# Optimization experiments

Hardware: AMD Instinct MI355X
Metric: run time of the kernel (lower is better)

The kernel has to match this reference:

```python
import jax, jax.numpy as jnp
import numpy as np

BATCH, SEQ_LEN, VOCAB, DIM = 64, 512, 32000, 512


def setup_inputs() -> dict:
    key = jax.random.key(0)
    k = jax.random.split(key, 6)
    s = 1.0 / np.sqrt(DIM)
    return {
        "x": jax.random.randint(k[0], (BATCH, SEQ_LEN), 0, VOCAB),
        "emb": jax.random.normal(k[1], (VOCAB, DIM), dtype=jnp.float32),
        "W_ih": jax.random.normal(k[2], (DIM, DIM), dtype=jnp.float32) * s,
        "W_hh": jax.random.normal(k[3], (DIM, DIM), dtype=jnp.float32) * s,
        "b_ih": jax.random.normal(k[4], (DIM,), dtype=jnp.float32) * s,
        "b_hh": jax.random.normal(k[5], (DIM,), dtype=jnp.float32) * s,
    }


def reference(x, emb, W_ih, W_hh, b_ih, b_hh):
    # Embedding lookup: [B, T, I]
    xe = emb[x]
    # Precompute input projections for all timesteps: [T, B, H]
    xp = jnp.einsum("bti,hi->tbh", xe, W_ih) + b_ih + b_hh
    h0 = jnp.zeros((x.shape[0], W_hh.shape[0]), dtype=xe.dtype)

    def step(h, xp_t):
        h_new = jnp.tanh(xp_t + h @ W_hh.T)
        return h_new, h_new

    _, hiddens = jax.lax.scan(step, h0, xp)  # [T, B, H]
    hiddens = jnp.transpose(hiddens, (1, 2, 0))  # [B, H, T]
    return jax.nn.softmax(hiddens, axis=1)
```

## Files before the change

kernel.cpp:

```cpp
#include <hip/hip_runtime.h>
#include <cstdint>

#define BATCH 64
#define SEQ   512
#define DIM   512
#define MTOT  (BATCH*SEQ)

#define CSL 8
#define GRP 32
#define RPG 2
#define SLOT (GRP*RPG*DIM)

__global__ __launch_bounds__(128) void pack_w(const float* __restrict__ W,
                                              float4* __restrict__ Wpk,
                                              unsigned long long* __restrict__ hpair) {
    const int c  = blockIdx.x;
    const int jb = threadIdx.x;
    const float4 v = *(const float4*)&W[(size_t)c * DIM + 4 * jb];
    Wpk[(size_t)jb * DIM + c] = v;
    hpair[(size_t)blockIdx.x * 128 + threadIdx.x] = 0ull;
}

__global__ __launch_bounds__(256) void embed_proj(
    const int*   __restrict__ xidx,
    const float* __restrict__ emb,
    const float* __restrict__ W_ih,
    const float* __restrict__ b_ih,
    const float* __restrict__ b_hh,
    float*       __restrict__ xp) {
    __shared__ float As[64][68];
    __shared__ float Bs[64][68];

    const int m0  = blockIdx.x * 64;
    const int n0  = blockIdx.y * 64;
    const int tid = threadIdx.x;

    const int lr = tid >> 4;
    const int lc = (tid & 15) << 2;

    int rows[4];
#pragma unroll
    for (int i = 0; i < 4; i++) rows[i] = xidx[m0 + lr + 16 * i];

    const int tm = (tid & 15) << 2;
    const int tn = (tid >> 4) << 2;

    float acc[4][4];
#pragma unroll
    for (int i = 0; i < 4; i++)
#pragma unroll
        for (int j = 0; j < 4; j++) acc[i][j] = 0.0f;

    for (int k0 = 0; k0 < DIM; k0 += 64) {
#pragma unroll
        for (int i = 0; i < 4; i++) {
            const int rl = lr + 16 * i;
            const float4 a = *(const float4*)&emb[(size_t)rows[i] * DIM + k0 + lc];
            As[lc + 0][rl] = a.x; As[lc + 1][rl] = a.y;
            As[lc + 2][rl] = a.z; As[lc + 3][rl] = a.w;
            const float4 b = *(const float4*)&W_ih[(size_t)(n0 + rl) * DIM + k0 + lc];
            Bs[lc + 0][rl] = b.x; Bs[lc + 1][rl] = b.y;
            Bs[lc + 2][rl] = b.z; Bs[lc + 3][rl] = b.w;
        }
        __syncthreads();
#pragma unroll 8
        for (int kk = 0; kk < 64; kk++) {
            const float4 a = *(const float4*)&As[kk][tm];
            const float4 b = *(const float4*)&Bs[kk][tn];
            acc[0][0] = fmaf(a.x, b.x, acc[0][0]);
            acc[0][1] = fmaf(a.x, b.y, acc[0][1]);
            acc[0][2] = fmaf(a.x, b.z, acc[0][2]);
            acc[0][3] = fmaf(a.x, b.w, acc[0][3]);
            acc[1][0] = fmaf(a.y, b.x, acc[1][0]);
            acc[1][1] = fmaf(a.y, b.y, acc[1][1]);
            acc[1][2] = fmaf(a.y, b.z, acc[1][2]);
            acc[1][3] = fmaf(a.y, b.w, acc[1][3]);
            acc[2][0] = fmaf(a.z, b.x, acc[2][0]);
            acc[2][1] = fmaf(a.z, b.y, acc[2][1]);
            acc[2][2] = fmaf(a.z, b.z, acc[2][2]);
            acc[2][3] = fmaf(a.z, b.w, acc[2][3]);
            acc[3][0] = fmaf(a.w, b.x, acc[3][0]);
            acc[3][1] = fmaf(a.w, b.y, acc[3][1]);
            acc[3][2] = fmaf(a.w, b.z, acc[3][2]);
            acc[3][3] = fmaf(a.w, b.w, acc[3][3]);
        }
        __syncthreads();
    }

    const int n = n0 + tn;
    const float bias0 = b_ih[n + 0] + b_hh[n + 0];
    const float bias1 = b_ih[n + 1] + b_hh[n + 1];
    const float bias2 = b_ih[n + 2] + b_hh[n + 2];
    const float bias3 = b_ih[n + 3] + b_hh[n + 3];
#pragma unroll
    for (int i = 0; i < 4; i++) {
        float4 o;
        o.x = acc[i][0] + bias0;
        o.y = acc[i][1] + bias1;
        o.z = acc[i][2] + bias2;
        o.w = acc[i][3] + bias3;
        *(float4*)&xp[(size_t)(m0 + tm + i) * DIM + n] = o;
    }
}

__global__ __launch_bounds__(512, 2)
void rnn_scan(const float4* __restrict__ Wpk, float* __restrict__ buf,
              unsigned long long* __restrict__ hpair) {
    __shared__ float hlds[RPG][DIM];
    __shared__ float part[2][RPG][8][64];

    const int tid   = threadIdx.x;
    const int slice = blockIdx.x / GRP;
    const int grp   = blockIdx.x % GRP;
    const int c     = tid & 63;
    const int ks    = tid >> 6;
    const int b0    = grp * RPG;
    const int col0  = slice * 64;
    const int hb    = ks * 16;

    float4 wreg[16];
#pragma unroll
    for (int i = 0; i < 16; i++)
        wreg[i] = Wpk[(size_t)(hb + i) * DIM + col0 + c];

    hlds[0][tid] = 0.0f;
    hlds[1][tid] = 0.0f;
    asm volatile("" ::: "memory");

    const unsigned long long* const pollb =
        hpair + (size_t)grp * (RPG * DIM) + tid;

    const int rr = tid >> 6;
    const int cc = tid & 63;
    float xq = 0.0f;
    size_t bufoff = 0;
    unsigned long long* pubp = nullptr;
    if (tid < 128) {
        bufoff = (size_t)(b0 + rr) * SEQ * DIM + col0 + cc;
        xq     = buf[bufoff];
        pubp   = hpair + ((size_t)grp * RPG + rr) * DIM + col0 + cc;
    }

    for (int t = 0; t < SEQ; t++) {
#pragma unroll
        for (int i = 0; i < 16; i++)
            asm volatile("" : "+v"(wreg[i].x), "+v"(wreg[i].y),
                              "+v"(wreg[i].z), "+v"(wreg[i].w));

        if (t > 0) {
            const unsigned long long* bp = pollb + (size_t)(t & 1) * SLOT;
            const unsigned tgt = (unsigned)t;
            unsigned long long v0 = __hip_atomic_load(bp, __ATOMIC_RELAXED,
                                                      __HIP_MEMORY_SCOPE_AGENT);
            unsigned long long v1 = __hip_atomic_load(bp + DIM, __ATOMIC_RELAXED,
                                                      __HIP_MEMORY_SCOPE_AGENT);
            int spins = 0;
            while (((unsigned)(v0 >> 32) != tgt) |
                   ((unsigned)(v1 >> 32) != tgt)) {
                if (++spins > 16) __builtin_amdgcn_s_sleep(1);
                v0 = __hip_atomic_load(bp, __ATOMIC_RELAXED,
                                       __HIP_MEMORY_SCOPE_AGENT);
                v1 = __hip_atomic_load(bp + DIM, __ATOMIC_RELAXED,
                                       __HIP_MEMORY_SCOPE_AGENT);
            }
            hlds[0][tid] = __uint_as_float((unsigned)v0);
            hlds[1][tid] = __uint_as_float((unsigned)v1);
            asm volatile("" ::: "memory");
        }

        float p0 = 0.f, p1 = 0.f;
        const float4* h40 = (const float4*)&hlds[0][0];
        const float4* h41 = (const float4*)&hlds[1][0];
#pragma unroll
        for (int i = 0; i < 16; i++) {
            const float4 w = wreg[i];
            const float4 a = h40[hb + i];
            const float4 b = h41[hb + i];
            p0 = fmaf(w.x, a.x, p0); p0 = fmaf(w.y, a.y, p0);
            p0 = fmaf(w.z, a.z, p0); p0 = fmaf(w.w, a.w, p0);
            p1 = fmaf(w.x, b.x, p1); p1 = fmaf(w.y, b.y, p1);
            p1 = fmaf(w.z, b.z, p1); p1 = fmaf(w.w, b.w, p1);
        }

        const int p = t & 1;
        part[p][0][ks][c] = p0;
        part[p][1][ks][c] = p1;
        __syncthreads();

        if (tid < 128) {
            float s = part[p][rr][0][cc];
#pragma unroll
            for (int k = 1; k < 8; k++) s += part[p][rr][k][cc];
            const float hn = tanhf(xq + s);
            if (t + 1 < SEQ) {
                const unsigned long long pv =
                    ((unsigned long long)(unsigned)(t + 1) << 32) |
                    (unsigned long long)__float_as_uint(hn);
                __hip_atomic_store(pubp + (size_t)((t + 1) & 1) * SLOT, pv,
                                   __ATOMIC_RELAXED, __HIP_MEMORY_SCOPE_AGENT);
            }
            buf[bufoff + (size_t)t * DIM] = hn;
            const int tn2 = (t + 1 < SEQ) ? (t + 1) : t;
            xq = buf[bufoff + (size_t)tn2 * DIM];
        }
    }
}

__global__ __launch_bounds__(256) void softmax_T(const float* __restrict__ hid,
                                                 float* __restrict__ out) {
    __shared__ float rowmax[64];
    __shared__ float rowinv[64];
    __shared__ float tile[64][65];

    const int b   = blockIdx.x;
    const int t0  = blockIdx.y * 64;
    const int tid = threadIdx.x;
    const float* base = hid + ((size_t)b * SEQ + t0) * DIM;

    const int r = tid >> 2;
    const int p = tid & 3;

    float m = -1e30f;
#pragma unroll 4
    for (int k = 0; k < 32; k++) {
        const float4 v = *(const float4*)&base[r * DIM + ((k * 4 + p) << 2)];
        m = fmaxf(m, fmaxf(fmaxf(v.x, v.y), fmaxf(v.z, v.w)));
    }
    m = fmaxf(m, __shfl_xor(m, 1));
    m = fmaxf(m, __shfl_xor(m, 2));

    float s = 0.0f;
#pragma unroll 4
    for (int k = 0; k < 32; k++) {
        const float4 v = *(const float4*)&base[r * DIM + ((k * 4 + p) << 2)];
        s += expf(v.x - m) + expf(v.y - m) + expf(v.z - m) + expf(v.w - m);
    }
    s += __shfl_xor(s, 1);
    s += __shfl_xor(s, 2);
    if (p == 0) {
        rowmax[r] = m;
        rowinv[r] = 1.0f / s;
    }
    __syncthreads();

    for (int hc = 0; hc < 8; hc++) {
#pragma unroll
        for (int i = 0; i < 16; i++) {
            const int lin = tid + 256 * i;
            const int rrr = lin >> 6;
            const int ccc = lin & 63;
            const float v = base[rrr * DIM + hc * 64 + ccc];
            tile[ccc][rrr] = expf(v - rowmax[rrr]) * rowinv[rrr];
        }
        __syncthreads();
#pragma unroll
        for (int i = 0; i < 16; i++) {
            const int lin = tid + 256 * i;
            const int hh  = lin >> 6;
            const int tt  = lin & 63;
            out[((size_t)b * DIM + hc * 64 + hh) * SEQ + t0 + tt] = tile[hh][tt];
        }
        __syncthreads();
    }
}

extern "C" void kernel_launch(void* const* d_in, const int* in_sizes, int n_in,
                              void* d_out, int out_size, void* d_ws, size_t ws_size,
                              hipStream_t stream) {
    const int*   x    = (const int*)  d_in[0];
    const float* emb  = (const float*)d_in[1];
    const float* W_ih = (const float*)d_in[2];
    const float* W_hh = (const float*)d_in[3];
    const float* b_ih = (const float*)d_in[4];
    const float* b_hh = (const float*)d_in[5];
    float* out = (float*)d_out;

    float* buf = (float*)d_ws;
    float4* Wpk = (float4*)out;
    unsigned long long* hpair =
        (unsigned long long*)(out + (4 << 20));

    pack_w<<<dim3(DIM), 128, 0, stream>>>(W_hh, Wpk, hpair);
    embed_proj<<<dim3(MTOT / 64, DIM / 64), 256, 0, stream>>>(x, emb, W_ih, b_ih, b_hh, buf);
    rnn_scan<<<CSL * GRP, 512, 0, stream>>>(Wpk, buf, hpair);
    softmax_T<<<dim3(BATCH, SEQ / 64), 256, 0, stream>>>(buf, out);
}
```

Baseline: 1.268 ms.

## Split RNN step per batch row to overlap row-B polling with row-A compute

```diff
diff --git a/kernel.cpp b/kernel.cpp
--- a/kernel.cpp
+++ b/kernel.cpp
@@ -107,7 +107,7 @@
 void rnn_scan(const float4* __restrict__ Wpk, float* __restrict__ buf,
               unsigned long long* __restrict__ hpair) {
     __shared__ float hlds[RPG][DIM];
-    __shared__ float part[2][RPG][8][64];
+    __shared__ float part[RPG][8][64];
 
     const int tid   = threadIdx.x;
     const int slice = blockIdx.x / GRP;
@@ -117,6 +117,7 @@
     const int b0    = grp * RPG;
     const int col0  = slice * 64;
     const int hb    = ks * 16;
+    const int wid   = ks;
 
     float4 wreg[16];
 #pragma unroll
@@ -127,70 +128,104 @@
     hlds[1][tid] = 0.0f;
     asm volatile("" ::: "memory");
 
-    const unsigned long long* const pollb =
-        hpair + (size_t)grp * (RPG * DIM) + tid;
-
-    const int rr = tid >> 6;
-    const int cc = tid & 63;
+    unsigned long long* const gbase = hpair + (size_t)grp * (RPG * DIM);
+
     float xq = 0.0f;
     size_t bufoff = 0;
     unsigned long long* pubp = nullptr;
-    if (tid < 128) {
-        bufoff = (size_t)(b0 + rr) * SEQ * DIM + col0 + cc;
+    if (wid < RPG) {
+        bufoff = (size_t)(b0 + wid) * SEQ * DIM + col0 + c;
         xq     = buf[bufoff];
-        pubp   = hpair + ((size_t)grp * RPG + rr) * DIM + col0 + cc;
-    }
+        pubp   = hpair + ((size_t)grp * RPG + wid) * DIM + col0 + c;
+    }
+
+    unsigned long long pendA = 0, pendB = 0;
 
     for (int t = 0; t < SEQ; t++) {
-#pragma unroll
-        for (int i = 0; i < 16; i++)
-            asm volatile("" : "+v"(wreg[i].x), "+v"(wreg[i].y),
-                              "+v"(wreg[i].z), "+v"(wreg[i].w));
+        const unsigned tgt = (unsigned)t;
 
         if (t > 0) {
-            const unsigned long long* bp = pollb + (size_t)(t & 1) * SLOT;
-            const unsigned tgt = (unsigned)t;
-            unsigned long long v0 = __hip_atomic_load(bp, __ATOMIC_RELAXED,
-                                                      __HIP_MEMORY_SCOPE_AGENT);
-            unsigned long long v1 = __hip_atomic_load(bp + DIM, __ATOMIC_RELAXED,
-                                                      __HIP_MEMORY_SCOPE_AGENT);
+            const unsigned long long* bp = gbase + (size_t)(t & 1) * SLOT + tid;
+            unsigned long long v = pendA;
             int spins = 0;
-            while (((unsigned)(v0 >> 32) != tgt) |
-                   ((unsigned)(v1 >> 32) != tgt)) {
+            while ((unsigned)(v >> 32) != tgt) {
                 if (++spins > 16) __builtin_amdgcn_s_sleep(1);
-                v0 = __hip_atomic_load(bp, __ATOMIC_RELAXED,
-                                       __HIP_MEMORY_SCOPE_AGENT);
-                v1 = __hip_atomic_load(bp + DIM, __ATOMIC_RELAXED,
-                                       __HIP_MEMORY_SCOPE_AGENT);
-            }
-            hlds[0][tid] = __uint_as_float((unsigned)v0);
-            hlds[1][tid] = __uint_as_float((unsigned)v1);
+                v = __hip_atomic_load(bp, __ATOMIC_RELAXED,
+                                      __HIP_MEMORY_SCOPE_AGENT);
+            }
+            hlds[0][tid] = __uint_as_float((unsigned)v);
             asm volatile("" ::: "memory");
-        }
-
-        float p0 = 0.f, p1 = 0.f;
-        const float4* h40 = (const float4*)&hlds[0][0];
-        const float4* h41 = (const float4*)&hlds[1][0];
-#pragma unroll
-        for (int i = 0; i < 16; i++) {
-            const float4 w = wreg[i];
-            const float4 a = h40[hb + i];
-            const float4 b = h41[hb + i];
-            p0 = fmaf(w.x, a.x, p0); p0 = fmaf(w.y, a.y, p0);
-            p0 = fmaf(w.z, a.z, p0); p0 = fmaf(w.w, a.w, p0);
-            p1 = fmaf(w.x, b.x, p1); p1 = fmaf(w.y, b.y, p1);
-            p1 = fmaf(w.z, b.z, p1); p1 = fmaf(w.w, b.w, p1);
-        }
-
-        const int p = t & 1;
-        part[p][0][ks][c] = p0;
-        part[p][1][ks][c] = p1;
-        __syncthreads();
-
-        if (tid < 128) {
-            float s = part[p][rr][0][cc];
-#pragma unroll
-            for (int k = 1; k < 8; k++) s += part[p][rr][k][cc];
+            pendB = __hip_atomic_load(bp + DIM, __ATOMIC_RELAXED,
+                                      __HIP_MEMORY_SCOPE_AGENT);
+        }
+
+        {
+            float p = 0.f;
+            const float4* h4 = (const float4*)&hlds[0][0];
+#pragma unroll
+            for (int i = 0; i < 16; i++) {
+                const float4 w = wreg[i];
+                const float4 a = h4[hb + i];
+                p = fmaf(w.x, a.x, p); p = fmaf(w.y, a.y, p);
+                p = fmaf(w.z, a.z, p); p = fmaf(w.w, a.w, p);
+            }
+            part[0][ks][c] = p;
+        }
+        __syncthreads();
+
+        if (wid == 0) {
+            float s = part[0][0][c];
+#pragma unroll
+            for (int k = 1; k < 8; k++) s += part[0][k][c];
+            const float hn = tanhf(xq + s);
+            if (t + 1 < SEQ) {
+                const unsigned long long pv =
+                    ((unsigned long long)(unsigned)(t + 1) << 32) |
+                    (unsigned long long)__float_as_uint(hn);
+                __hip_atomic_store(pubp + (size_t)((t + 1) & 1) * SLOT, pv,
+                                   __ATOMIC_RELAXED, __HIP_MEMORY_SCOPE_AGENT);
+            }
+            buf[bufoff + (size_t)t * DIM] = hn;
+            const int tn2 = (t + 1 < SEQ) ? (t + 1) : t;
+            xq = buf[bufoff + (size_t)tn2 * DIM];
+        }
+
+        if (t > 0) {
+            const unsigned long long* bp =
+                gbase + (size_t)(t & 1) * SLOT + DIM + tid;
+            unsigned long long v = pendB;
+            int spins = 0;
+            while ((unsigned)(v >> 32) != tgt) {
+                if (++spins > 16) __builtin_amdgcn_s_sleep(1);
+                v = __hip_atomic_load(bp, __ATOMIC_RELAXED,
+                                      __HIP_MEMORY_SCOPE_AGENT);
+            }
+            hlds[1][tid] = __uint_as_float((unsigned)v);
+            asm volatile("" ::: "memory");
+        }
+
+        {
+            float p = 0.f;
+            const float4* h4 = (const float4*)&hlds[1][0];
+#pragma unroll
+            for (int i = 0; i < 16; i++) {
+                const float4 w = wreg[i];
+                const float4 a = h4[hb + i];
+                p = fmaf(w.x, a.x, p); p = fmaf(w.y, a.y, p);
+                p = fmaf(w.z, a.z, p); p = fmaf(w.w, a.w, p);
+            }
+            part[1][ks][c] = p;
+        }
+        if (t + 1 < SEQ)
+            pendA = __hip_atomic_load(
+                gbase + (size_t)((t + 1) & 1) * SLOT + tid,
+                __ATOMIC_RELAXED, __HIP_MEMORY_SCOPE_AGENT);
+        __syncthreads();
+
+        if (wid == 1) {
+            float s = part[1][0][c];
+#pragma unroll
+            for (int k = 1; k < 8; k++) s += part[1][k][c];
             const float hn = tanhf(xq + s);
             if (t + 1 < SEQ) {
                 const unsigned long long pv =
```

After: 1.269 ms. Within noise of the previous version (+0.1%).

## Repartition RNN scan into 16 column slices and pipeline rows per block

Applied to the files above, without the earlier changes.

```diff
diff --git a/kernel.cpp b/kernel.cpp
--- a/kernel.cpp
+++ b/kernel.cpp
@@ -6,9 +6,9 @@
 #define DIM   512
 #define MTOT  (BATCH*SEQ)
 
-#define CSL 8
-#define GRP 32
-#define RPG 2
+#define CSL 16
+#define GRP 16
+#define RPG 4
 #define SLOT (GRP*RPG*DIM)
 
 __global__ __launch_bounds__(128) void pack_w(const float* __restrict__ W,
@@ -106,102 +106,123 @@
 __global__ __launch_bounds__(512, 2)
 void rnn_scan(const float4* __restrict__ Wpk, float* __restrict__ buf,
               unsigned long long* __restrict__ hpair) {
-    __shared__ float hlds[RPG][DIM];
-    __shared__ float part[2][RPG][8][64];
+    __shared__ float    hlds[DIM];
+    __shared__ float    part[2][RPG][8][32];
+    __shared__ unsigned done_[RPG][8];
 
     const int tid   = threadIdx.x;
     const int slice = blockIdx.x / GRP;
     const int grp   = blockIdx.x % GRP;
-    const int c     = tid & 63;
-    const int ks    = tid >> 6;
+    const int c     = tid & 31;
+    const int z     = tid >> 5;
+    const int wv    = tid >> 6;
+    const int lane  = tid & 63;
     const int b0    = grp * RPG;
-    const int col0  = slice * 64;
-    const int hb    = ks * 16;
-
-    float4 wreg[16];
-#pragma unroll
-    for (int i = 0; i < 16; i++)
-        wreg[i] = Wpk[(size_t)(hb + i) * DIM + col0 + c];
-
-    hlds[0][tid] = 0.0f;
-    hlds[1][tid] = 0.0f;
-    asm volatile("" ::: "memory");
-
-    const unsigned long long* const pollb =
-        hpair + (size_t)grp * (RPG * DIM) + tid;
-
-    const int rr = tid >> 6;
-    const int cc = tid & 63;
+    const int col0  = slice * 32;
+
+    if (tid < RPG * 8) ((unsigned*)done_)[tid] = 0u;
+    hlds[tid] = 0.0f;
+    __syncthreads();
+
+    float4 wr[8];
+    {
+        const float4* wp = Wpk + (size_t)(8 * z) * DIM + col0 + c;
+#pragma unroll
+        for (int i = 0; i < 8; i++)
+            asm volatile("global_load_dwordx4 %0, %1, off"
+                         : "=v"(wr[i]) : "v"(wp + (size_t)i * DIM));
+        asm volatile("s_waitcnt vmcnt(0)" ::: "memory");
+        __builtin_amdgcn_sched_barrier(0);
+    }
+
+    unsigned long long* const pbase = hpair + (size_t)grp * (RPG * DIM);
+
+    size_t bufr = 0;
+    unsigned long long* pubp = nullptr;
     float xq = 0.0f;
-    size_t bufoff = 0;
-    unsigned long long* pubp = nullptr;
-    if (tid < 128) {
-        bufoff = (size_t)(b0 + rr) * SEQ * DIM + col0 + cc;
-        xq     = buf[bufoff];
-        pubp   = hpair + ((size_t)grp * RPG + rr) * DIM + col0 + cc;
-    }
+    if (wv < RPG && lane < 32) {
+        bufr = (size_t)(b0 + wv) * SEQ * DIM + col0 + c;
+        xq   = buf[bufr];
+        pubp = hpair + ((size_t)grp * RPG + wv) * DIM + col0 + c;
+    }
+
+    unsigned long long pend[4] = {0ull, 0ull, 0ull, 0ull};
 
     for (int t = 0; t < SEQ; t++) {
 #pragma unroll
-        for (int i = 0; i < 16; i++)
-            asm volatile("" : "+v"(wreg[i].x), "+v"(wreg[i].y),
-                              "+v"(wreg[i].z), "+v"(wreg[i].w));
-
-        if (t > 0) {
-            const unsigned long long* bp = pollb + (size_t)(t & 1) * SLOT;
-            const unsigned tgt = (unsigned)t;
-            unsigned long long v0 = __hip_atomic_load(bp, __ATOMIC_RELAXED,
-                                                      __HIP_MEMORY_SCOPE_AGENT);
-            unsigned long long v1 = __hip_atomic_load(bp + DIM, __ATOMIC_RELAXED,
-                                                      __HIP_MEMORY_SCOPE_AGENT);
-            int spins = 0;
-            while (((unsigned)(v0 >> 32) != tgt) |
-                   ((unsigned)(v1 >> 32) != tgt)) {
-                if (++spins > 16) __builtin_amdgcn_s_sleep(1);
-                v0 = __hip_atomic_load(bp, __ATOMIC_RELAXED,
-                                       __HIP_MEMORY_SCOPE_AGENT);
-                v1 = __hip_atomic_load(bp + DIM, __ATOMIC_RELAXED,
-                                       __HIP_MEMORY_SCOPE_AGENT);
+        for (int p = 0; p < RPG; p++) {
+            if (t > 0) {
+                const unsigned tgt = (unsigned)t;
+                unsigned long long v = pend[p];
+                if ((unsigned)(v >> 32) != tgt) {
+                    const unsigned long long* sp =
+                        pbase + (size_t)(t & 1) * SLOT + p * DIM + tid;
+                    int spins = 0;
+                    do {
+                        if (++spins > 16) __builtin_amdgcn_s_sleep(1);
+                        v = __hip_atomic_load(sp, __ATOMIC_RELAXED,
+                                              __HIP_MEMORY_SCOPE_AGENT);
+                    } while ((unsigned)(v >> 32) != tgt);
+                }
+                hlds[tid] = __uint_as_float((unsigned)v);
+                asm volatile("" ::: "memory");
             }
-            hlds[0][tid] = __uint_as_float((unsigned)v0);
-            hlds[1][tid] = __uint_as_float((unsigned)v1);
-            asm volatile("" ::: "memory");
-        }
-
-        float p0 = 0.f, p1 = 0.f;
-        const float4* h40 = (const float4*)&hlds[0][0];
-        const float4* h41 = (const float4*)&hlds[1][0];
-#pragma unroll
-        for (int i = 0; i < 16; i++) {
-            const float4 w = wreg[i];
-            const float4 a = h40[hb + i];
-            const float4 b = h41[hb + i];
-            p0 = fmaf(w.x, a.x, p0); p0 = fmaf(w.y, a.y, p0);
-            p0 = fmaf(w.z, a.z, p0); p0 = fmaf(w.w, a.w, p0);
-            p1 = fmaf(w.x, b.x, p1); p1 = fmaf(w.y, b.y, p1);
-            p1 = fmaf(w.z, b.z, p1); p1 = fmaf(w.w, b.w, p1);
-        }
-
-        const int p = t & 1;
-        part[p][0][ks][c] = p0;
-        part[p][1][ks][c] = p1;
-        __syncthreads();
-
-        if (tid < 128) {
-            float s = part[p][rr][0][cc];
-#pragma unroll
-            for (int k = 1; k < 8; k++) s += part[p][rr][k][cc];
-            const float hn = tanhf(xq + s);
-            if (t + 1 < SEQ) {
-                const unsigned long long pv =
-                    ((unsigned long long)(unsigned)(t + 1) << 32) |
-                    (unsigned long long)__float_as_uint(hn);
-                __hip_atomic_store(pubp + (size_t)((t + 1) & 1) * SLOT, pv,
-                                   __ATOMIC_RELAXED, __HIP_MEMORY_SCOPE_AGENT);
+
+            {
+                const float4* hz = (const float4*)hlds + 8 * z;
+                float4 a = make_float4(0.f, 0.f, 0.f, 0.f);
+#pragma unroll
+                for (int i = 0; i < 8; i++) {
+                    const float4 w = wr[i];
+                    const float4 h = hz[i];
+                    a.x = fmaf(w.x, h.x, a.x);
+                    a.y = fmaf(w.y, h.y, a.y);
+                    a.z = fmaf(w.z, h.z, a.z);
+                    a.w = fmaf(w.w, h.w, a.w);
+                }
+                float s = (a.x + a.y) + (a.z + a.w);
+                s += __shfl_xor(s, 32);
+                if (lane < 32) part[t & 1][p][wv][c] = s;
+                if (lane == 0)
+                    __hip_atomic_store(&done_[p][wv], (unsigned)(t + 1),
+                                       __ATOMIC_RELEASE,
+                                       __HIP_MEMORY_SCOPE_WORKGROUP);
             }
-            buf[bufoff + (size_t)t * DIM] = hn;
-            const int tn2 = (t + 1 < SEQ) ? (t + 1) : t;
-            xq = buf[bufoff + (size_t)tn2 * DIM];
+
+            {
+                const int r2 = (p + 2) & 3;
+                const int tl = t + ((p + 2) >> 2);
+                pend[r2] = __hip_atomic_load(
+                    pbase + (size_t)(tl & 1) * SLOT + r2 * DIM + tid,
+                    __ATOMIC_RELAXED, __HIP_MEMORY_SCOPE_AGENT);
+            }
+
+            if (wv == p && lane < 32) {
+                const unsigned want = (unsigned)(t + 1);
+                int sp_ = 0;
+                while (true) {
+                    const unsigned st = __hip_atomic_load(
+                        &done_[p][lane & 7], __ATOMIC_ACQUIRE,
+                        __HIP_MEMORY_SCOPE_WORKGROUP);
+                    if (__all(st >= want)) break;
+                    if ((++sp_ & 3) == 0) __builtin_amdgcn_s_sleep(1);
+                }
+                const int q = t & 1;
+                float s = part[q][p][0][c];
+#pragma unroll
+                for (int k = 1; k < 8; k++) s += part[q][p][k][c];
+                const float hn = tanhf(xq + s);
+                if (t + 1 < SEQ) {
+                    const unsigned long long pv =
+                        ((unsigned long long)(unsigned)(t + 1) << 32) |
+                        (unsigned long long)__float_as_uint(hn);
+                    __hip_atomic_store(pubp + (size_t)((t + 1) & 1) * SLOT, pv,
+                                       __ATOMIC_RELAXED, __HIP_MEMORY_SCOPE_AGENT);
+                }
+                buf[bufr + (size_t)t * DIM] = hn;
+                const int tn2 = (t + 1 < SEQ) ? (t + 1) : t;
+                xq = buf[bufr + (size_t)tn2 * DIM];
+            }
         }
     }
 }
```

New measurement: 2.040 ms. 60.9% more time.
